# Kernel optimization log

Hardware: AMD Instinct MI355X
Metric: run time of the kernel (lower is better)

Reference implementation:

```python
import jax, jax.numpy as jnp
import numpy as np

B, S, D = 4, 4096, 64

def setup_inputs() -> dict:
    key = jax.random.key(0)
    kq, kk, kv = jax.random.split(key, 3)
    q = jax.random.normal(kq, (B, S, D), dtype=jnp.float32)
    k = jax.random.normal(kk, (B, S, D), dtype=jnp.float32)
    v = jax.random.normal(kv, (B, S, D), dtype=jnp.float32)
    return {"q": q, "k": k, "v": v}

def reference(q, k, v):
    d_k = k.shape[-1]
    # scores: [B, S, S]
    scores = jnp.einsum('bqd,bkd->bqk', q, k) / jnp.sqrt(jnp.asarray(d_k, q.dtype))
    s = scores.shape[-1]
    # causal mask: disallow j > i (strict upper triangle)
    causal = jnp.tril(jnp.ones((scores.shape[-2], s), dtype=bool))
    scores = jnp.where(causal, scores, jnp.asarray(-jnp.inf, scores.dtype))
    norm_scores = jax.nn.softmax(scores, axis=-1)
    return jnp.einsum('bqk,bkd->bqd', norm_scores, v)
```

## Files before the change

kernel.cpp:

```cpp
#include <hip/hip_runtime.h>

#define B_ 4
#define S_ 4096
#define D_ 64

typedef __attribute__((ext_vector_type(8))) short short8;
typedef __attribute__((ext_vector_type(4))) float f32x4;
typedef __attribute__((ext_vector_type(4))) int int4v;
typedef __attribute__((ext_vector_type(2))) unsigned uint2v;
typedef unsigned short u16;

__device__ __forceinline__ unsigned pack_bf2(float a, float b) {
  unsigned ua = __float_as_uint(a) + 0x8000u;
  unsigned ub = __float_as_uint(b) + 0x8000u;
  return __builtin_amdgcn_perm(ub, ua, 0x07060302);
}

__global__ __launch_bounds__(256) void cvt_all_k(const float* __restrict__ q,
                                                 const float* __restrict__ k,
                                                 const float* __restrict__ v,
                                                 u16* __restrict__ wsQ,
                                                 u16* __restrict__ wsK,
                                                 u16* __restrict__ wsV) {
  int blk = blockIdx.x;
  if (blk < 1024) {
    const float* src = (blk < 512) ? q : k;
    u16* dst = (blk < 512) ? wsQ : wsK;
    float scale = (blk < 512) ? 0.18033688011112042f : 1.0f;
    int t = ((blk & 511) << 8) + threadIdx.x;
    const f32x4* s4 = (const f32x4*)src;
    f32x4 a = s4[2 * t], b = s4[2 * t + 1];
    int4v r;
    r[0] = (int)pack_bf2(a[0] * scale, a[1] * scale);
    r[1] = (int)pack_bf2(a[2] * scale, a[3] * scale);
    r[2] = (int)pack_bf2(b[0] * scale, b[1] * scale);
    r[3] = (int)pack_bf2(b[2] * scale, b[3] * scale);
    *(int4v*)(dst + 8 * (long)t) = r;
  } else {
    int t = ((blk - 1024) << 8) + threadIdx.x;
    int lane = t & 63;
    int rest = t >> 6;
    int js = rest & 1;  rest >>= 1;
    int nb = rest & 3;  rest >>= 2;
    int c64 = rest & 63;
    int b = rest >> 6;
    int cc = lane & 15, gg = lane >> 4;
    int row = c64 * 64 + js * 32 + gg * 8;
    int d = nb * 16 + cc;
    const float* src = v + ((long)(b * S_ + row)) * D_ + d;
    float e[8];
#pragma unroll
    for (int i = 0; i < 8; i++) e[i] = src[(long)i * D_];
    int4v r;
    r[0] = (int)pack_bf2(e[0], e[1]);
    r[1] = (int)pack_bf2(e[2], e[3]);
    r[2] = (int)pack_bf2(e[4], e[5]);
    r[3] = (int)pack_bf2(e[6], e[7]);
    *(int4v*)(wsV + 8 * (long)t) = r;
  }
}

#define MFMA(a, bb, cc) __builtin_amdgcn_mfma_f32_16x16x32_bf16((a), (bb), (cc), 0, 0, 0)

__global__ __launch_bounds__(512, 2) void attn_k(const u16* __restrict__ wsQ,
                                                 const u16* __restrict__ wsK,
                                                 const u16* __restrict__ wsV,
                                                 float* __restrict__ out) {
  int bid = blockIdx.x;
  int b   = bid & 3;
  int g32 = 127 - (bid >> 2);
  int tid = threadIdx.x;
  int w = tid >> 6, lane = tid & 63, c = lane & 15, g4 = lane >> 4;
  int cmax = g32 >> 1;

  __shared__ float sMem[8][1152];
  __shared__ float sML[8][2][16];

  float* wbase = &sMem[w][0];

  short8 qf0[2], qf1[2];
#pragma unroll
  for (int t = 0; t < 2; t++) {
    const u16* qp = wsQ + ((long)(b * S_ + g32 * 32 + t * 16 + c)) * D_ + g4 * 8;
    qf0[t] = *(const short8*)qp;
    qf1[t] = *(const short8*)(qp + 32);
  }
  f32x4 zz = {0.f, 0.f, 0.f, 0.f};
  float lp[2] = {0.f, 0.f};
  f32x4 o[2][4];
#pragma unroll
  for (int t = 0; t < 2; t++)
#pragma unroll
    for (int n = 0; n < 4; n++) o[t][n] = zz;

  for (int ck = w; ck <= cmax; ck += 8) {
    const u16* kp = wsK + ((long)(b * S_ + ck * 64 + c)) * D_ + g4 * 8;
    short8 kf[8];
#pragma unroll
    for (int jb = 0; jb < 4; jb++) {
      kf[jb * 2]     = *(const short8*)(kp + jb * 1024);
      kf[jb * 2 + 1] = *(const short8*)(kp + jb * 1024 + 32);
    }
    const u16* vp = wsV + ((long)((b * 64 + ck) * 8 * 64 + lane)) * 8;
    short8 vf[8];
#pragma unroll
    for (int i = 0; i < 8; i++) vf[i] = *(const short8*)(vp + 512 * i);

#pragma unroll
    for (int t = 0; t < 2; t++) {
      f32x4 s0 = MFMA(kf[0], qf0[t], zz); s0 = MFMA(kf[1], qf1[t], s0);
      f32x4 s1 = MFMA(kf[2], qf0[t], zz); s1 = MFMA(kf[3], qf1[t], s1);
      f32x4 s2 = MFMA(kf[4], qf0[t], zz); s2 = MFMA(kf[5], qf1[t], s2);
      f32x4 s3 = MFMA(kf[6], qf0[t], zz); s3 = MFMA(kf[7], qf1[t], s3);

      if (ck == cmax) {
        int qq = (g32 * 32 + 16 * t - 64 * cmax) + c;
        int j0 = g4 * 4;
#pragma unroll
        for (int r2 = 0; r2 < 4; r2++) {
          if (j0 + r2      > qq) s0[r2] = -1e30f;
          if (j0 + 16 + r2 > qq) s1[r2] = -1e30f;
          if (j0 + 32 + r2 > qq) s2[r2] = -1e30f;
          if (j0 + 48 + r2 > qq) s3[r2] = -1e30f;
        }
      }

      float sum = 0.f;
#pragma unroll
      for (int r2 = 0; r2 < 4; r2++) {
        s0[r2] = exp2f(s0[r2]); sum += s0[r2];
        s1[r2] = exp2f(s1[r2]); sum += s1[r2];
        s2[r2] = exp2f(s2[r2]); sum += s2[r2];
        s3[r2] = exp2f(s3[r2]); sum += s3[r2];
      }
      lp[t] += sum;

      float* P = wbase + (t & 1) * 576;
      uint2v w0 = {pack_bf2(s0[0], s0[1]), pack_bf2(s0[2], s0[3])};
      uint2v w1 = {pack_bf2(s1[0], s1[1]), pack_bf2(s1[2], s1[3])};
      uint2v w2 = {pack_bf2(s2[0], s2[1]), pack_bf2(s2[2], s2[3])};
      uint2v w3 = {pack_bf2(s3[0], s3[1]), pack_bf2(s3[2], s3[3])};
      *(uint2v*)&P[c * 36 + 2 * g4]      = w0;
      *(uint2v*)&P[c * 36 + 2 * g4 + 8]  = w1;
      *(uint2v*)&P[c * 36 + 2 * g4 + 16] = w2;
      *(uint2v*)&P[c * 36 + 2 * g4 + 24] = w3;
      short8 p0 = *(const short8*)&P[c * 36 + 4 * g4];
      short8 p1 = *(const short8*)&P[c * 36 + 16 + 4 * g4];
      o[t][0] = MFMA(vf[0], p0, o[t][0]); o[t][0] = MFMA(vf[1], p1, o[t][0]);
      o[t][1] = MFMA(vf[2], p0, o[t][1]); o[t][1] = MFMA(vf[3], p1, o[t][1]);
      o[t][2] = MFMA(vf[4], p0, o[t][2]); o[t][2] = MFMA(vf[5], p1, o[t][2]);
      o[t][3] = MFMA(vf[6], p0, o[t][3]); o[t][3] = MFMA(vf[7], p1, o[t][3]);
    }
  }

#pragma unroll
  for (int t = 0; t < 2; t++) {
    float lt = lp[t];
    lt += __shfl_xor(lt, 16);
    lt += __shfl_xor(lt, 32);
    if (g4 == 0) sML[w][t][c] = lt;
  }

  for (int t = 0; t < 2; t++) {
    __syncthreads();
#pragma unroll
    for (int n = 0; n < 4; n++)
      *(f32x4*)&wbase[c * 68 + n * 16 + g4 * 4] = o[t][n];
    __syncthreads();

    if (tid < 256) {
      int q = tid >> 4, d4 = tid & 15;
      float L = 0.f;
      f32x4 acc = {0.f, 0.f, 0.f, 0.f};
#pragma unroll
      for (int w2 = 0; w2 < 8; w2++) {
        L += sML[w2][t][q];
        f32x4 pv = *(f32x4*)&sMem[w2][q * 68 + d4 * 4];
#pragma unroll
        for (int i = 0; i < 4; i++) acc[i] += pv[i];
      }
      float inv = 1.f / L;
      f32x4 r;
#pragma unroll
      for (int i = 0; i < 4; i++) r[i] = acc[i] * inv;
      *(f32x4*)(out + ((long)(b * S_ + g32 * 32 + t * 16 + q)) * D_ + d4 * 4) = r;
    }
  }
}

extern "C" void kernel_launch(void* const* d_in, const int* in_sizes, int n_in,
                              void* d_out, int out_size, void* d_ws, size_t ws_size,
                              hipStream_t stream) {
  const float* q = (const float*)d_in[0];
  const float* k = (const float*)d_in[1];
  const float* v = (const float*)d_in[2];
  float* out = (float*)d_out;

  u16* wsQ = (u16*)d_ws;
  u16* wsK = wsQ + (long)B_ * S_ * D_;
  u16* wsV = wsK + (long)B_ * S_ * D_;

  cvt_all_k<<<1536, 256, 0, stream>>>(q, k, v, wsQ, wsK, wsV);
  attn_k<<<512, 512, 0, stream>>>(wsQ, wsK, wsV, out);
}
```

Before: 94.06 us.

## Switch attention MFMAs to 32x32x16 bf16 tiles with matching V layout

Replaces the 16x16x32 MFMA tiling, which used two 16-row query subtiles per wave, with 32x32x16 MFMAs that cover all 32 queries at once. The V conversion layout, the P staging through LDS and the final cross-wave reduction are rearranged to fit the new fragment layout, and the epilogue now does one reduction pass using all 512 threads. The aim is fewer MFMA instructions, fewer P round trips through LDS and fewer barriers. The cost is larger accumulator tiles (two f32x16) per wave, which may raise register pressure.

```diff
diff --git a/kernel.cpp b/kernel.cpp
--- a/kernel.cpp
+++ b/kernel.cpp
@@ -6,6 +6,7 @@
 
 typedef __attribute__((ext_vector_type(8))) short short8;
 typedef __attribute__((ext_vector_type(4))) float f32x4;
+typedef __attribute__((ext_vector_type(16))) float f32x16;
 typedef __attribute__((ext_vector_type(4))) int int4v;
 typedef __attribute__((ext_vector_type(2))) unsigned uint2v;
 typedef unsigned short u16;
@@ -39,15 +40,13 @@
   } else {
     int t = ((blk - 1024) << 8) + threadIdx.x;
     int lane = t & 63;
-    int rest = t >> 6;
-    int js = rest & 1;  rest >>= 1;
-    int nb = rest & 3;  rest >>= 2;
-    int c64 = rest & 63;
-    int b = rest >> 6;
-    int cc = lane & 15, gg = lane >> 4;
-    int row = c64 * 64 + js * 32 + gg * 8;
-    int d = nb * 16 + cc;
-    const float* src = v + ((long)(b * S_ + row)) * D_ + d;
+    int J  = (t >> 6) & 3;
+    int dt = (t >> 8) & 1;
+    int ck = (t >> 9) & 63;
+    int b  = t >> 15;
+    int row = ck * 64 + J * 16 + (lane >> 5) * 8;
+    int col = dt * 32 + (lane & 31);
+    const float* src = v + ((long)(b * S_ + row)) * D_ + col;
     float e[8];
 #pragma unroll
     for (int i = 0; i < 8; i++) e[i] = src[(long)i * D_];
@@ -60,7 +59,7 @@
   }
 }
 
-#define MFMA(a, bb, cc) __builtin_amdgcn_mfma_f32_16x16x32_bf16((a), (bb), (cc), 0, 0, 0)
+#define MFMA32(a, bb, cc) __builtin_amdgcn_mfma_f32_32x32x16_bf16((a), (bb), (cc), 0, 0, 0)
 
 __global__ __launch_bounds__(512, 2) void attn_k(const u16* __restrict__ wsQ,
                                                  const u16* __restrict__ wsK,
@@ -70,122 +69,117 @@
   int b   = bid & 3;
   int g32 = 127 - (bid >> 2);
   int tid = threadIdx.x;
-  int w = tid >> 6, lane = tid & 63, c = lane & 15, g4 = lane >> 4;
+  int w = tid >> 6, lane = tid & 63, c2 = lane & 31, h = lane >> 5;
   int cmax = g32 >> 1;
+  int q0 = g32 * 32;
 
-  __shared__ float sMem[8][1152];
-  __shared__ float sML[8][2][16];
+  __shared__ float sMem[8][2176];
+  __shared__ float sML[8][32];
 
-  float* wbase = &sMem[w][0];
+  float* W = &sMem[w][0];
 
-  short8 qf0[2], qf1[2];
+  short8 qf[4];
 #pragma unroll
-  for (int t = 0; t < 2; t++) {
-    const u16* qp = wsQ + ((long)(b * S_ + g32 * 32 + t * 16 + c)) * D_ + g4 * 8;
-    qf0[t] = *(const short8*)qp;
-    qf1[t] = *(const short8*)(qp + 32);
-  }
-  f32x4 zz = {0.f, 0.f, 0.f, 0.f};
-  float lp[2] = {0.f, 0.f};
-  f32x4 o[2][4];
+  for (int kk = 0; kk < 4; kk++)
+    qf[kk] = *(const short8*)(wsQ + ((long)(b * S_ + q0 + c2)) * D_ + kk * 16 + h * 8);
+
+  f32x16 o0 = {0.f}, o1 = {0.f};
 #pragma unroll
-  for (int t = 0; t < 2; t++)
-#pragma unroll
-    for (int n = 0; n < 4; n++) o[t][n] = zz;
+  for (int r = 0; r < 16; r++) { o0[r] = 0.f; o1[r] = 0.f; }
+  float lp = 0.f;
 
   for (int ck = w; ck <= cmax; ck += 8) {
-    const u16* kp = wsK + ((long)(b * S_ + ck * 64 + c)) * D_ + g4 * 8;
-    short8 kf[8];
+    const u16* kp = wsK + ((long)(b * S_ + ck * 64 + c2)) * D_ + h * 8;
+    short8 kf[2][4];
 #pragma unroll
-    for (int jb = 0; jb < 4; jb++) {
-      kf[jb * 2]     = *(const short8*)(kp + jb * 1024);
-      kf[jb * 2 + 1] = *(const short8*)(kp + jb * 1024 + 32);
+    for (int jt = 0; jt < 2; jt++)
+#pragma unroll
+      for (int kk = 0; kk < 4; kk++)
+        kf[jt][kk] = *(const short8*)(kp + jt * 32 * D_ + kk * 16);
+    const u16* vp = wsV + ((long)(b * 64 + ck)) * 4096 + (long)lane * 8;
+    short8 vf[2][4];
+#pragma unroll
+    for (int dt = 0; dt < 2; dt++)
+#pragma unroll
+      for (int J = 0; J < 4; J++)
+        vf[dt][J] = *(const short8*)(vp + (dt * 4 + J) * 512);
+
+    f32x16 s[2];
+#pragma unroll
+    for (int r = 0; r < 16; r++) { s[0][r] = 0.f; s[1][r] = 0.f; }
+#pragma unroll
+    for (int kk = 0; kk < 4; kk++) {
+      s[0] = MFMA32(kf[0][kk], qf[kk], s[0]);
+      s[1] = MFMA32(kf[1][kk], qf[kk], s[1]);
     }
-    const u16* vp = wsV + ((long)((b * 64 + ck) * 8 * 64 + lane)) * 8;
-    short8 vf[8];
+
+    if (ck == cmax) {
+      int dq = 32 * (g32 & 1) + c2;
 #pragma unroll
-    for (int i = 0; i < 8; i++) vf[i] = *(const short8*)(vp + 512 * i);
+      for (int r = 0; r < 16; r++) {
+        int row = (r & 3) + 8 * (r >> 2) + 4 * h;
+        if (row      > dq) s[0][r] = -1e30f;
+        if (row + 32 > dq) s[1][r] = -1e30f;
+      }
+    }
+
+    float sum = 0.f;
+#pragma unroll
+    for (int r = 0; r < 16; r++) {
+      s[0][r] = exp2f(s[0][r]); sum += s[0][r];
+      s[1][r] = exp2f(s[1][r]); sum += s[1][r];
+    }
+    lp += sum;
 
 #pragma unroll
-    for (int t = 0; t < 2; t++) {
-      f32x4 s0 = MFMA(kf[0], qf0[t], zz); s0 = MFMA(kf[1], qf1[t], s0);
-      f32x4 s1 = MFMA(kf[2], qf0[t], zz); s1 = MFMA(kf[3], qf1[t], s1);
-      f32x4 s2 = MFMA(kf[4], qf0[t], zz); s2 = MFMA(kf[5], qf1[t], s2);
-      f32x4 s3 = MFMA(kf[6], qf0[t], zz); s3 = MFMA(kf[7], qf1[t], s3);
+    for (int jt = 0; jt < 2; jt++)
+#pragma unroll
+      for (int grp = 0; grp < 4; grp++) {
+        uint2v dw = {pack_bf2(s[jt][4 * grp],     s[jt][4 * grp + 1]),
+                     pack_bf2(s[jt][4 * grp + 2], s[jt][4 * grp + 3])};
+        *(uint2v*)&W[c2 * 36 + 16 * jt + 4 * grp + 2 * h] = dw;
+      }
+    short8 p[4];
+#pragma unroll
+    for (int J = 0; J < 4; J++)
+      p[J] = *(const short8*)&W[c2 * 36 + 8 * J + 4 * h];
 
-      if (ck == cmax) {
-        int qq = (g32 * 32 + 16 * t - 64 * cmax) + c;
-        int j0 = g4 * 4;
 #pragma unroll
-        for (int r2 = 0; r2 < 4; r2++) {
-          if (j0 + r2      > qq) s0[r2] = -1e30f;
-          if (j0 + 16 + r2 > qq) s1[r2] = -1e30f;
-          if (j0 + 32 + r2 > qq) s2[r2] = -1e30f;
-          if (j0 + 48 + r2 > qq) s3[r2] = -1e30f;
-        }
-      }
-
-      float sum = 0.f;
-#pragma unroll
-      for (int r2 = 0; r2 < 4; r2++) {
-        s0[r2] = exp2f(s0[r2]); sum += s0[r2];
-        s1[r2] = exp2f(s1[r2]); sum += s1[r2];
-        s2[r2] = exp2f(s2[r2]); sum += s2[r2];
-        s3[r2] = exp2f(s3[r2]); sum += s3[r2];
-      }
-      lp[t] += sum;
-
-      float* P = wbase + (t & 1) * 576;
-      uint2v w0 = {pack_bf2(s0[0], s0[1]), pack_bf2(s0[2], s0[3])};
-      uint2v w1 = {pack_bf2(s1[0], s1[1]), pack_bf2(s1[2], s1[3])};
-      uint2v w2 = {pack_bf2(s2[0], s2[1]), pack_bf2(s2[2], s2[3])};
-      uint2v w3 = {pack_bf2(s3[0], s3[1]), pack_bf2(s3[2], s3[3])};
-      *(uint2v*)&P[c * 36 + 2 * g4]      = w0;
-      *(uint2v*)&P[c * 36 + 2 * g4 + 8]  = w1;
-      *(uint2v*)&P[c * 36 + 2 * g4 + 16] = w2;
-      *(uint2v*)&P[c * 36 + 2 * g4 + 24] = w3;
-      short8 p0 = *(const short8*)&P[c * 36 + 4 * g4];
-      short8 p1 = *(const short8*)&P[c * 36 + 16 + 4 * g4];
-      o[t][0] = MFMA(vf[0], p0, o[t][0]); o[t][0] = MFMA(vf[1], p1, o[t][0]);
-      o[t][1] = MFMA(vf[2], p0, o[t][1]); o[t][1] = MFMA(vf[3], p1, o[t][1]);
-      o[t][2] = MFMA(vf[4], p0, o[t][2]); o[t][2] = MFMA(vf[5], p1, o[t][2]);
-      o[t][3] = MFMA(vf[6], p0, o[t][3]); o[t][3] = MFMA(vf[7], p1, o[t][3]);
+    for (int J = 0; J < 4; J++) {
+      o0 = MFMA32(vf[0][J], p[J], o0);
+      o1 = MFMA32(vf[1][J], p[J], o1);
     }
   }
 
+  lp += __shfl_xor(lp, 32);
+  if (h == 0) sML[w][c2] = lp;
 #pragma unroll
-  for (int t = 0; t < 2; t++) {
-    float lt = lp[t];
-    lt += __shfl_xor(lt, 16);
-    lt += __shfl_xor(lt, 32);
-    if (g4 == 0) sML[w][t][c] = lt;
+  for (int dt = 0; dt < 2; dt++)
+#pragma unroll
+    for (int grp = 0; grp < 4; grp++) {
+      f32x4 t4;
+      const f32x16& ov = dt ? o1 : o0;
+      t4[0] = ov[4 * grp]; t4[1] = ov[4 * grp + 1];
+      t4[2] = ov[4 * grp + 2]; t4[3] = ov[4 * grp + 3];
+      *(f32x4*)&W[c2 * 68 + 32 * dt + 8 * grp + 4 * h] = t4;
+    }
+  __syncthreads();
+
+  int q = tid >> 4, d4 = tid & 15;
+  float L = 0.f;
+  f32x4 acc = {0.f, 0.f, 0.f, 0.f};
+#pragma unroll
+  for (int w2 = 0; w2 < 8; w2++) {
+    L += sML[w2][q];
+    f32x4 pv = *(f32x4*)&sMem[w2][q * 68 + d4 * 4];
+#pragma unroll
+    for (int i = 0; i < 4; i++) acc[i] += pv[i];
   }
-
-  for (int t = 0; t < 2; t++) {
-    __syncthreads();
+  float inv = 1.f / L;
+  f32x4 r;
 #pragma unroll
-    for (int n = 0; n < 4; n++)
-      *(f32x4*)&wbase[c * 68 + n * 16 + g4 * 4] = o[t][n];
-    __syncthreads();
-
-    if (tid < 256) {
-      int q = tid >> 4, d4 = tid & 15;
-      float L = 0.f;
-      f32x4 acc = {0.f, 0.f, 0.f, 0.f};
-#pragma unroll
-      for (int w2 = 0; w2 < 8; w2++) {
-        L += sML[w2][t][q];
-        f32x4 pv = *(f32x4*)&sMem[w2][q * 68 + d4 * 4];
-#pragma unroll
-        for (int i = 0; i < 4; i++) acc[i] += pv[i];
-      }
-      float inv = 1.f / L;
-      f32x4 r;
-#pragma unroll
-      for (int i = 0; i < 4; i++) r[i] = acc[i] * inv;
-      *(f32x4*)(out + ((long)(b * S_ + g32 * 32 + t * 16 + q)) * D_ + d4 * 4) = r;
-    }
-  }
+  for (int i = 0; i < 4; i++) r[i] = acc[i] * inv;
+  *(f32x4*)(out + ((long)(b * S_ + q0 + q)) * D_ + d4 * 4) = r;
 }
 
 extern "C" void kernel_launch(void* const* d_in, const int* in_sizes, int n_in,
```

Measured after the change: 92.36 us. Within noise of the previous version (-1.8%).
